# Kernel tuning notes

Measured on AMD Instinct MI355X. Metric: run time of the kernel, lower is better.

The kernel has to match this reference:

```python
import jax, jax.numpy as jnp
import numpy as np

# YOLOv5-style NMS + scale_coords constants
CONF_THRES = 0.25
IOU_THRES = 0.45
MAX_DET = 300      # max detections kept per image
TOPK = 1024        # candidate pool fed to greedy NMS (static for jit)
MAX_WH = 4096.0    # class offset for class-aware NMS
IMG1 = (640.0, 640.0)   # shape1: letterboxed network input (h, w)
IMG0 = (720.0, 1280.0)  # shape0: original image (h, w)


def xywh2xyxy(x):
    xy, wh = x[..., :2], x[..., 2:4] * 0.5
    return jnp.concatenate([xy - wh, xy + wh], axis=-1)


def iou_one_to_many(b, B):
    # b: [4], B: [K,4] in xyxy
    lt = jnp.maximum(b[:2], B[:, :2])
    rb = jnp.minimum(b[2:], B[:, 2:])
    wh = jnp.clip(rb - lt, 0.0)
    inter = wh[:, 0] * wh[:, 1]
    a1 = (b[2] - b[0]) * (b[3] - b[1])
    a2 = (B[:, 2] - B[:, 0]) * (B[:, 3] - B[:, 1])
    return inter / (a1 + a2 - inter + 1e-9)


def nms_single(pred):
    # pred: [N, 85] = xywh, obj, 80 class scores
    obj = pred[:, 4]
    conf_all = obj[:, None] * pred[:, 5:]          # obj * cls conf
    conf = conf_all.max(axis=-1)
    cls = jnp.argmax(conf_all, axis=-1).astype(pred.dtype)
    boxes = xywh2xyxy(pred[:, :4])
    valid = (obj > CONF_THRES) & (conf > CONF_THRES)
    sc = jnp.where(valid, conf, -1.0)
    sc_top, idx = jax.lax.top_k(sc, TOPK)          # candidate pool
    b = boxes[idx]                                  # [K,4]
    c = cls[idx]                                    # [K]
    off = b + c[:, None] * MAX_WH                   # class-aware offset boxes

    def body(i, state):
        s, sel, selv = state
        p = jnp.argmax(s)
        pv = s[p] > 0.0
        iou = iou_one_to_many(off[p], off)
        s = jnp.where(iou > IOU_THRES, -1.0, s).at[p].set(-1.0)
        return s, sel.at[i].set(p), selv.at[i].set(pv)

    init = (sc_top, jnp.zeros(MAX_DET, jnp.int32), jnp.zeros(MAX_DET, bool))
    _, sel, selv = jax.lax.fori_loop(0, MAX_DET, body, init)

    det = jnp.concatenate(
        [b[sel], sc_top[sel][:, None], c[sel][:, None]], axis=-1)  # [max_det,6]
    return jnp.where(selv[:, None], det, 0.0)


def scale_coords(coords):
    # undo letterbox: IMG1 (h1,w1) -> IMG0 (h0,w0)
    h1, w1 = IMG1
    h0, w0 = IMG0
    gain = min(h1 / h0, w1 / w0)
    pad_x = (w1 - w0 * gain) / 2.0
    pad_y = (h1 - h0 * gain) / 2.0
    x1 = jnp.clip((coords[..., 0] - pad_x) / gain, 0.0, w0)
    y1 = jnp.clip((coords[..., 1] - pad_y) / gain, 0.0, h0)
    x2 = jnp.clip((coords[..., 2] - pad_x) / gain, 0.0, w0)
    y2 = jnp.clip((coords[..., 3] - pad_y) / gain, 0.0, h0)
    return jnp.stack([x1, y1, x2, y2], axis=-1)


def setup_inputs() -> dict:
    key = jax.random.key(0)
    kxy, kwh, kobj, kcls = jax.random.split(key, 4)
    B, N, NC = 16, 25200, 80
    xy = jax.random.uniform(kxy, (B, N, 2), jnp.float32) * 640.0
    wh = jax.random.uniform(kwh, (B, N, 2), jnp.float32) * 160.0 + 2.0
    obj = jax.random.uniform(kobj, (B, N, 1), jnp.float32)
    cls = jax.random.uniform(kcls, (B, N, NC), jnp.float32)
    pred = jnp.concatenate([xy, wh, obj, cls], axis=-1)  # [B, N, 85]
    return {"pred": pred}


def reference(pred):
    det = jax.vmap(nms_single)(pred)                 # [B, max_det, 6]
    boxes = scale_coords(det[..., :4])
    # columns: x1,y1,x2,y2 (rescaled), score, label
    return jnp.concatenate([boxes, det[..., 4:]], axis=-1)
```

## Files before the change

kernel.cpp:

```cpp
#include <hip/hip_runtime.h>
#include <stdint.h>

#define N_CAND 25200
#define NB 16
#define ROW 85
#define TK 1024
#define MAXDET 300
#define CAP 2048
#define BITS_LO 0x3E800000u
#define TRI_WORDS 7680

typedef unsigned long long u64;
typedef unsigned int u32;

static __device__ __forceinline__ u64 u64min(u64 a, u64 b) { return a < b ? a : b; }
static __device__ __forceinline__ u64 u64max(u64 a, u64 b) { return a > b ? a : b; }
static __device__ __forceinline__ int triBase(int w) { return 64 * (15 * w - (w * (w - 1)) / 2); }

__global__ __launch_bounds__(256) void score_kernel(const float* __restrict__ pred,
                                                    u64* __restrict__ keys)
{
#pragma clang fp contract(off)
    __shared__ float tile[64 * ROW];
    const int tid = threadIdx.x;
    const int row0 = blockIdx.x * 64;
    const float4* src = (const float4*)(pred + (size_t)row0 * ROW);
    float4* dst = (float4*)tile;
#pragma unroll
    for (int i = 0; i < 6; ++i) {
        int idx = tid + (i << 8);
        if (idx < (64 * ROW) / 4) dst[idx] = src[idx];
    }
    __syncthreads();

    const int r = tid >> 2, sub = tid & 3;
    const float* rowp = tile + r * ROW;
    const float obj = rowp[4];
    const int base = 5 + sub * 20;
    float bv = obj * rowp[base];
    int bi = base - 5;
#pragma unroll
    for (int c = 1; c < 20; ++c) {
        float p = obj * rowp[base + c];
        if (p > bv) { bv = p; bi = base - 5 + c; }
    }
#pragma unroll
    for (int off = 1; off <= 2; off <<= 1) {
        float ov = __shfl_xor(bv, off, 64);
        int   oi = __shfl_xor(bi, off, 64);
        if (ov > bv || (ov == bv && oi < bi)) { bv = ov; bi = oi; }
    }
    if (sub == 0) {
        int w = row0 + r;
        u32 n = (u32)w % N_CAND;
        u64 key = 0;
        if (obj > 0.25f && bv > 0.25f)
            key = ((u64)__float_as_uint(bv) << 32) | (((u64)(25199u - n)) << 7) | (u32)bi;
        keys[w] = key;
    }
}

__global__ __launch_bounds__(1024) void topk_kernel(const float* __restrict__ pred,
                                                    const u64* __restrict__ keys,
                                                    float4* __restrict__ soaA,
                                                    float4* __restrict__ soaB)
{
#pragma clang fp contract(off)
    __shared__ u64 sbuf[CAP];
    __shared__ u32 histA[2048];
    __shared__ u32 histB[2048];
    __shared__ u32 s_t;
    __shared__ int s_cnt;

    const int tid = threadIdx.x;
    const int b = blockIdx.x;
    const u64* kb = keys + (size_t)b * N_CAND;
    const float* pb = pred + (size_t)b * N_CAND * ROW;

    for (int i = tid; i < 2048; i += 1024) histA[i] = 0;
    if (tid == 0) { s_cnt = 0; s_t = 0; }
    __syncthreads();

    for (int n = tid; n < N_CAND; n += 1024) {
        u32 bits = (u32)(kb[n] >> 32);
        if (bits) {
            int bin = (int)((bits - BITS_LO) >> 13);
            bin = bin < 0 ? 0 : (bin > 2047 ? 2047 : bin);
            atomicAdd(&histA[bin], 1u);
        }
    }
    __syncthreads();

    u32* srcp = histA; u32* dstp = histB;
    for (int step = 1; step < 2048; step <<= 1) {
        for (int i = tid; i < 2048; i += 1024)
            dstp[i] = srcp[i] + ((i + step < 2048) ? srcp[i + step] : 0u);
        __syncthreads();
        u32* t = srcp; srcp = dstp; dstp = t;
    }
    for (int i = tid; i < 2048; i += 1024) {
        u32 S = srcp[i];
        if (S >= TK && (i == 2047 || srcp[i + 1] < TK)) s_t = (u32)i;
    }
    __syncthreads();
    const u32 thr = BITS_LO + (s_t << 13);

    for (int n = tid; n < N_CAND; n += 1024) {
        u64 k = kb[n];
        if ((u32)(k >> 32) >= thr) {
            int pos = atomicAdd(&s_cnt, 1);
            if (pos < CAP) sbuf[pos] = k;
        }
    }
    __syncthreads();
    int cnt = s_cnt; if (cnt > CAP) cnt = CAP;
    for (int i = tid; i < CAP; i += 1024) if (i >= cnt) sbuf[i] = 0ull;
    __syncthreads();

    {
        const int E0 = tid << 1;
        u64 e0 = sbuf[E0], e1 = sbuf[E0 + 1];
        for (int k = 2; k <= CAP; k <<= 1) {
            for (int j = k >> 1; j > 0; j >>= 1) {
                const bool asc = ((E0 & k) == 0);
                if (j >= 128) {
                    __syncthreads();
                    sbuf[E0] = e0; sbuf[E0 + 1] = e1;
                    __syncthreads();
                    u64 p0 = sbuf[E0 ^ j], p1 = sbuf[(E0 + 1) ^ j];
                    const bool low = ((E0 & j) == 0);
                    e0 = (asc == low) ? u64min(e0, p0) : u64max(e0, p0);
                    e1 = (asc == low) ? u64min(e1, p1) : u64max(e1, p1);
                } else if (j >= 2) {
                    const int l = j >> 1;
                    u64 p0 = __shfl_xor(e0, l, 64);
                    u64 p1 = __shfl_xor(e1, l, 64);
                    const bool low = ((E0 & j) == 0);
                    e0 = (asc == low) ? u64min(e0, p0) : u64max(e0, p0);
                    e1 = (asc == low) ? u64min(e1, p1) : u64max(e1, p1);
                } else {
                    u64 mn = u64min(e0, e1), mx = u64max(e0, e1);
                    e0 = asc ? mn : mx;
                    e1 = asc ? mx : mn;
                }
            }
        }
        __syncthreads();
        sbuf[E0] = e0; sbuf[E0 + 1] = e1;
        __syncthreads();
    }

    {
        const int i = tid;
        u64 k = sbuf[CAP - 1 - i];
        u32 bits = (u32)(k >> 32);
        float4 A, Bv;
        if (bits) {
            u32 lo = (u32)k;
            u32 n = 25199u - (lo >> 7);
            float c = (float)(lo & 127u);
            const float* rp = pb + (size_t)n * ROW;
            float x = rp[0], y = rp[1], ww = rp[2], hh = rp[3];
            float hw = ww * 0.5f, hv = hh * 0.5f;
            float x1 = x - hw, y1 = y - hv, x2 = x + hw, y2 = y + hv;
            float offc = c * 4096.0f;
            float area = ((x2 + offc) - (x1 + offc)) * ((y2 + offc) - (y1 + offc));
            A = make_float4(x1, y1, x2, y2);
            Bv = make_float4(area, __uint_as_float(bits), c, 0.0f);
        } else {
            A = make_float4(0.0f, 0.0f, 0.0f, 0.0f);
            Bv = make_float4(0.0f, -1.0f, 0.0f, 0.0f);
        }
        soaA[b * TK + i] = A;
        soaB[b * TK + i] = Bv;
    }
}

__global__ __launch_bounds__(512) void mask_kernel(const float4* __restrict__ soaA,
                                                   const float4* __restrict__ soaB,
                                                   u64* __restrict__ tri,
                                                   u64* __restrict__ diagArr)
{
#pragma clang fp contract(off)
    __shared__ float4 cA[TK];
    __shared__ float4 cB[TK];
    const int tid = threadIdx.x;
    const int b = blockIdx.y;
    const int wi = blockIdx.x;
    const int rbase = wi << 6;
    for (int i = tid; i < TK; i += 512) { cA[i] = soaA[b * TK + i]; cB[i] = soaB[b * TK + i]; }
    __syncthreads();

    u64* trib = tri + (size_t)b * TRI_WORDS;
    const int Bw = triBase(wi);
    const int s = 15 - wi;

    const int wave = tid >> 6, lane = tid & 63;
    for (int rr = 0; rr < 8; ++rr) {
        int i = rbase + (wave << 3) + rr;
        int r = i & 63;
        float4 P = cA[i]; float4 Pb = cB[i];
        float offp = Pb.z * 4096.0f;
        float px1 = P.x + offp, py1 = P.y + offp, px2 = P.z + offp, py2 = P.w + offp;
        float parea = Pb.x;
        u64 myword = 0;
        for (int word = wi; word < 16; ++word) {
            int j = (word << 6) + lane;
            float4 Q = cA[j]; float4 Qb = cB[j];
            float offj = Qb.z * 4096.0f;
            float qx1 = Q.x + offj, qy1 = Q.y + offj, qx2 = Q.z + offj, qy2 = Q.w + offj;
            float ltx = fmaxf(px1, qx1), lty = fmaxf(py1, qy1);
            float rbx = fminf(px2, qx2), rby = fminf(py2, qy2);
            float w2 = fmaxf(rbx - ltx, 0.0f), h2 = fmaxf(rby - lty, 0.0f);
            float inter = w2 * h2;
            float iou = inter / (parea + Qb.x - inter + 1e-9f);
            u64 m = __ballot(iou > 0.45f);
            if (lane == word) myword = m;
        }
        if (lane == wi) diagArr[(b << 10) + i] = myword;
        else if (lane > wi && lane < 16) trib[Bw + r * s + (lane - wi - 1)] = myword;
    }
}

__global__ __launch_bounds__(1024) void sweep_kernel(const float4* __restrict__ soaA,
                                                     const float4* __restrict__ soaB,
                                                     const u64* __restrict__ tri,
                                                     const u64* __restrict__ diagArr,
                                                     float* __restrict__ out)
{
#pragma clang fp contract(off)
    __shared__ u64 tri_lds[TRI_WORDS];
    __shared__ int sel[MAXDET];
    __shared__ int s_nsel;
    const int tid = threadIdx.x;
    const int b = blockIdx.x;

    const u64* gtri = tri + (size_t)b * TRI_WORDS;
    for (int i = tid; i < TRI_WORDS; i += 1024) tri_lds[i] = gtri[i];
    __syncthreads();

    if (tid < 64) {
        const int lane = tid;
        const u64* db = diagArr + (b << 10);

        int nv = TK;
        for (int k = 0; k < 16; ++k) {
            float s = soaB[b * TK + (k << 6) + lane].y;
            u64 m = __ballot(s > 0.0f);
            if (m != ~0ull) { nv = (k << 6) + (int)__builtin_ctzll(~m); break; }
        }

        u64 removed = 0;
        int nsel = 0;
        const int g = lane >> 4;
        const int word = lane & 15;
        u64 diag = db[lane];
        for (int w = 0; w < 16; ++w) {
            u64 dnext = (w < 15) ? db[((w + 1) << 6) + lane] : 0ull;
            u64 wv = __shfl(removed, w, 64);
            int rem = nv - (w << 6);
            u64 validm = (rem >= 64) ? ~0ull : ((rem <= 0) ? 0ull : ((1ull << rem) - 1ull));
            u64 alive = validm & ~wv;
            u64 selbits = 0;
            while (alive != 0ull && nsel < MAXDET) {
                int i = (int)__builtin_ctzll(alive);
                if (lane == 0) sel[nsel] = (w << 6) + i;
                ++nsel;
                selbits |= (1ull << i);
                u64 d = __shfl(diag, i, 64);
                alive &= ~d;
                alive &= ~(1ull << i);
            }
            if (selbits != 0ull && w < 15) {
                const int Bw = triBase(w);
                const int s = 15 - w;
                u64 sb = selbits;
                if (g >= 1 && sb) sb &= sb - 1;
                if (g >= 2 && sb) sb &= sb - 1;
                if (g >= 3 && sb) sb &= sb - 1;
                u64 acc = 0;
                while (sb) {
                    int i = (int)__builtin_ctzll(sb);
                    if (word > w) acc |= tri_lds[Bw + i * s + (word - w - 1)];
                    sb &= sb - 1; if (sb) { sb &= sb - 1; if (sb) { sb &= sb - 1; if (sb) sb &= sb - 1; } }
                }
                acc |= __shfl_xor(acc, 16, 64);
                acc |= __shfl_xor(acc, 32, 64);
                removed |= acc;
            }
            diag = dnext;
            if (nsel >= MAXDET || rem <= 64) break;
        }
        if (lane == 0) s_nsel = nsel;
    }
    __syncthreads();

    const int nsel = s_nsel;
    for (int r = tid; r < MAXDET; r += 1024) {
        float* o = out + ((size_t)b * MAXDET + r) * 6;
        if (r < nsel) {
            int p = sel[r];
            float4 A = soaA[b * TK + p];
            float4 Bv = soaB[b * TK + p];
            float X1 = (A.x - 0.0f) / 0.5f;
            float Y1 = (A.y - 140.0f) / 0.5f;
            float X2 = (A.z - 0.0f) / 0.5f;
            float Y2 = (A.w - 140.0f) / 0.5f;
            X1 = fminf(fmaxf(X1, 0.0f), 1280.0f);
            Y1 = fminf(fmaxf(Y1, 0.0f), 720.0f);
            X2 = fminf(fmaxf(X2, 0.0f), 1280.0f);
            Y2 = fminf(fmaxf(Y2, 0.0f), 720.0f);
            o[0] = X1; o[1] = Y1; o[2] = X2; o[3] = Y2;
            o[4] = Bv.y; o[5] = Bv.z;
        } else {
            o[0] = 0.0f; o[1] = 0.0f; o[2] = 0.0f;
            o[3] = 0.0f; o[4] = 0.0f; o[5] = 0.0f;
        }
    }
}

extern "C" void kernel_launch(void* const* d_in, const int* in_sizes, int n_in,
                              void* d_out, int out_size, void* d_ws, size_t ws_size,
                              hipStream_t stream)
{
    const float* pred = (const float*)d_in[0];
    float* out = (float*)d_out;

    u64* keys = (u64*)d_ws;
    u64* tri = (u64*)d_ws;
    u64* diagArr = (u64*)((char*)d_ws + 983040);
    float4* soaA = (float4*)((char*)d_ws + 3225600);
    float4* soaB = (float4*)((char*)d_ws + 3225600 + 262144);

    score_kernel<<<(NB * N_CAND) / 64, 256, 0, stream>>>(pred, keys);
    topk_kernel<<<NB, 1024, 0, stream>>>(pred, keys, soaA, soaB);
    mask_kernel<<<dim3(16, NB), 512, 0, stream>>>(soaA, soaB, tri, diagArr);
    sweep_kernel<<<NB, 1024, 0, stream>>>(soaA, soaB, tri, diagArr, out);
}
```

Baseline: 133.6 us.

## Bucket top-k by histogram bins, split mask rows, async LDS loads

The top-k selection now scatters candidates into per-bin offsets from the histogram prefix sum and sorts each small bin with a wave-level bitonic network. This replaces the 2048-element block-wide bitonic sort, which is kept only as a fallback when a bin holds more than 64 entries. The mask kernel precomputes class-offset coordinates into SoA shared arrays and launches twice as many blocks, each covering half a word row. The score kernel uses direct global-to-LDS loads and an occupancy hint. The changes add complexity and a data-dependent fallback path.

```diff
diff --git a/kernel.cpp b/kernel.cpp
--- a/kernel.cpp
+++ b/kernel.cpp
@@ -17,8 +17,8 @@
 static __device__ __forceinline__ u64 u64max(u64 a, u64 b) { return a > b ? a : b; }
 static __device__ __forceinline__ int triBase(int w) { return 64 * (15 * w - (w * (w - 1)) / 2); }
 
-__global__ __launch_bounds__(256) void score_kernel(const float* __restrict__ pred,
-                                                    u64* __restrict__ keys)
+__global__ __launch_bounds__(256, 8) void score_kernel(const float* __restrict__ pred,
+                                                       u64* __restrict__ keys)
 {
 #pragma clang fp contract(off)
     __shared__ float tile[64 * ROW];
@@ -29,7 +29,12 @@
 #pragma unroll
     for (int i = 0; i < 6; ++i) {
         int idx = tid + (i << 8);
-        if (idx < (64 * ROW) / 4) dst[idx] = src[idx];
+        if (idx < (64 * ROW) / 4) {
+            __builtin_amdgcn_global_load_lds(
+                (const __attribute__((address_space(1))) void*)(src + idx),
+                (__attribute__((address_space(3))) void*)(dst + idx),
+                16, 0, 0);
+        }
     }
     __syncthreads();
 
@@ -70,7 +75,7 @@
     __shared__ u32 histA[2048];
     __shared__ u32 histB[2048];
     __shared__ u32 s_t;
-    __shared__ int s_cnt;
+    __shared__ int s_fb;
 
     const int tid = threadIdx.x;
     const int b = blockIdx.x;
@@ -78,7 +83,8 @@
     const float* pb = pred + (size_t)b * N_CAND * ROW;
 
     for (int i = tid; i < 2048; i += 1024) histA[i] = 0;
-    if (tid == 0) { s_cnt = 0; s_t = 0; }
+    for (int i = tid; i < CAP; i += 1024) sbuf[i] = 0ull;
+    if (tid == 0) { s_t = 0; s_fb = 0; }
     __syncthreads();
 
     for (int n = tid; n < N_CAND; n += 1024) {
@@ -103,21 +109,49 @@
         if (S >= TK && (i == 2047 || srcp[i + 1] < TK)) s_t = (u32)i;
     }
     __syncthreads();
-    const u32 thr = BITS_LO + (s_t << 13);
+    const int t = (int)s_t;
+    const u32 thr = BITS_LO + ((u32)t << 13);
+
+    for (int i = tid; i < 2048; i += 1024) {
+        u32 base = (i < 2047) ? srcp[i + 1] : 0u;
+        dstp[i] = base;
+        if (i >= t && (srcp[i] - base) > 64u) s_fb = 1;
+    }
+    __syncthreads();
 
     for (int n = tid; n < N_CAND; n += 1024) {
         u64 k = kb[n];
-        if ((u32)(k >> 32) >= thr) {
-            int pos = atomicAdd(&s_cnt, 1);
+        u32 bits = (u32)(k >> 32);
+        if (bits >= thr) {
+            int bin = (int)((bits - BITS_LO) >> 13);
+            bin = bin < 0 ? 0 : (bin > 2047 ? 2047 : bin);
+            u32 pos = atomicAdd(&dstp[bin], 1u);
             if (pos < CAP) sbuf[pos] = k;
         }
     }
     __syncthreads();
-    int cnt = s_cnt; if (cnt > CAP) cnt = CAP;
-    for (int i = tid; i < CAP; i += 1024) if (i >= cnt) sbuf[i] = 0ull;
-    __syncthreads();
-
-    {
+
+    if (!s_fb) {
+        const int wave = tid >> 6, lane = tid & 63;
+        for (int bin = t + wave; bin < 2048; bin += 16) {
+            u32 base = (bin < 2047) ? srcp[bin + 1] : 0u;
+            u32 end = srcp[bin]; if (end > CAP) end = CAP;
+            if (end <= base + 1) continue;
+            u32 cnt_b = end - base;
+            u64 v = (lane < (int)cnt_b) ? sbuf[base + lane] : 0ull;
+#pragma unroll
+            for (int k2 = 2; k2 <= 64; k2 <<= 1) {
+                for (int j = k2 >> 1; j > 0; j >>= 1) {
+                    u64 p = __shfl_xor(v, j, 64);
+                    const bool up = ((lane & k2) == 0);
+                    const bool low = ((lane & j) == 0);
+                    v = (up == low) ? u64max(v, p) : u64min(v, p);
+                }
+            }
+            if (lane < (int)cnt_b) sbuf[base + lane] = v;
+        }
+        __syncthreads();
+    } else {
         const int E0 = tid << 1;
         u64 e0 = sbuf[E0], e1 = sbuf[E0 + 1];
         for (int k = 2; k <= CAP; k <<= 1) {
@@ -152,7 +186,7 @@
 
     {
         const int i = tid;
-        u64 k = sbuf[CAP - 1 - i];
+        u64 k = sbuf[s_fb ? (CAP - 1 - i) : i];
         u32 bits = (u32)(k >> 32);
         float4 A, Bv;
         if (bits) {
@@ -182,13 +216,19 @@
                                                    u64* __restrict__ diagArr)
 {
 #pragma clang fp contract(off)
-    __shared__ float4 cA[TK];
-    __shared__ float4 cB[TK];
+    __shared__ float qx1[TK], qy1[TK], qx2[TK], qy2[TK], qar[TK];
     const int tid = threadIdx.x;
     const int b = blockIdx.y;
-    const int wi = blockIdx.x;
-    const int rbase = wi << 6;
-    for (int i = tid; i < TK; i += 512) { cA[i] = soaA[b * TK + i]; cB[i] = soaB[b * TK + i]; }
+    const int rbase = blockIdx.x * 32;
+    const int wi = rbase >> 6;
+    for (int i = tid; i < TK; i += 512) {
+        float4 A = soaA[b * TK + i];
+        float4 Bv = soaB[b * TK + i];
+        float off = Bv.z * 4096.0f;
+        qx1[i] = A.x + off; qy1[i] = A.y + off;
+        qx2[i] = A.z + off; qy2[i] = A.w + off;
+        qar[i] = Bv.x;
+    }
     __syncthreads();
 
     u64* trib = tri + (size_t)b * TRI_WORDS;
@@ -196,24 +236,20 @@
     const int s = 15 - wi;
 
     const int wave = tid >> 6, lane = tid & 63;
-    for (int rr = 0; rr < 8; ++rr) {
-        int i = rbase + (wave << 3) + rr;
+    for (int rr = 0; rr < 4; ++rr) {
+        int i = rbase + (wave << 2) + rr;
         int r = i & 63;
-        float4 P = cA[i]; float4 Pb = cB[i];
-        float offp = Pb.z * 4096.0f;
-        float px1 = P.x + offp, py1 = P.y + offp, px2 = P.z + offp, py2 = P.w + offp;
-        float parea = Pb.x;
+        float px1 = qx1[i], py1 = qy1[i];
+        float px2 = qx2[i], py2 = qy2[i];
+        float parea = qar[i];
         u64 myword = 0;
         for (int word = wi; word < 16; ++word) {
             int j = (word << 6) + lane;
-            float4 Q = cA[j]; float4 Qb = cB[j];
-            float offj = Qb.z * 4096.0f;
-            float qx1 = Q.x + offj, qy1 = Q.y + offj, qx2 = Q.z + offj, qy2 = Q.w + offj;
-            float ltx = fmaxf(px1, qx1), lty = fmaxf(py1, qy1);
-            float rbx = fminf(px2, qx2), rby = fminf(py2, qy2);
+            float ltx = fmaxf(px1, qx1[j]), lty = fmaxf(py1, qy1[j]);
+            float rbx = fminf(px2, qx2[j]), rby = fminf(py2, qy2[j]);
             float w2 = fmaxf(rbx - ltx, 0.0f), h2 = fmaxf(rby - lty, 0.0f);
             float inter = w2 * h2;
-            float iou = inter / (parea + Qb.x - inter + 1e-9f);
+            float iou = inter / (parea + qar[j] - inter + 1e-9f);
             u64 m = __ballot(iou > 0.45f);
             if (lane == word) myword = m;
         }
@@ -334,6 +370,6 @@
 
     score_kernel<<<(NB * N_CAND) / 64, 256, 0, stream>>>(pred, keys);
     topk_kernel<<<NB, 1024, 0, stream>>>(pred, keys, soaA, soaB);
-    mask_kernel<<<dim3(16, NB), 512, 0, stream>>>(soaA, soaB, tri, diagArr);
+    mask_kernel<<<dim3(32, NB), 512, 0, stream>>>(soaA, soaB, tri, diagArr);
     sweep_kernel<<<NB, 1024, 0, stream>>>(soaA, soaB, tri, diagArr, out);
 }
```

After: 126.4 us. 5.4% less time.
